# Optimization experiments

Measured on AMD Instinct MI355X. Metric: run time of the kernel, lower is better.

## Reference

```python
import math
import jax, jax.numpy as jnp
import numpy as np

B, LQ, LK, D, H = 4, 2048, 2048, 512, 8  # dim_Q=dim_K=dim_V=D, num_heads=H


def _layernorm(x, g, b, eps=1e-5):
    mu = jnp.mean(x, axis=-1, keepdims=True)
    var = jnp.var(x, axis=-1, keepdims=True)
    return (x - mu) * jax.lax.rsqrt(var + eps) * g + b


def setup_inputs() -> dict:
    key = jax.random.key(0)
    ks = jax.random.split(key, 16)
    s = 1.0 / math.sqrt(D)
    return {
        "Q": jax.random.normal(ks[0], (B, LQ, D), jnp.float32),
        "K": jax.random.normal(ks[1], (B, LK, D), jnp.float32),
        "pad_mask": jax.random.randint(ks[2], (B, LK), 0, 2, jnp.int32),
        "Wq": jax.random.normal(ks[3], (D, D), jnp.float32) * s,
        "bq": jnp.zeros((D,), jnp.float32),
        "Wk": jax.random.normal(ks[4], (D, D), jnp.float32) * s,
        "bk": jnp.zeros((D,), jnp.float32),
        "Wv": jax.random.normal(ks[5], (D, D), jnp.float32) * s,
        "bv": jnp.zeros((D,), jnp.float32),
        "Wo": jax.random.normal(ks[6], (D, D), jnp.float32) * s,
        "bo": jnp.zeros((D,), jnp.float32),
        "g0": jnp.ones((D,), jnp.float32),
        "b0": jnp.zeros((D,), jnp.float32),
        "g1": jnp.ones((D,), jnp.float32),
        "b1": jnp.zeros((D,), jnp.float32),
    }


def reference(Q, K, pad_mask, Wq, bq, Wk, bk, Wv, bv, Wo, bo, g0, b0, g1, b1):
    d = D // H  # head dim (torch: split(dim_split, 2) then cat along batch)
    Qh = (Q @ Wq + bq).reshape(B, LQ, H, d)
    Kh = (K @ Wk + bk).reshape(B, LK, H, d)
    Vh = (K @ Wv + bv).reshape(B, LK, H, d)
    # NOTE: original scales by sqrt(dim_V), not sqrt(head_dim)
    score = jnp.einsum('bqhd,bkhd->bhqk', Qh, Kh) / np.float32(math.sqrt(D))
    m = pad_mask[:, None, None, :].astype(score.dtype)  # (B,1,1,Lk)
    score = jnp.where(m == 0, jnp.float32(-1e12), score)
    A = jax.nn.softmax(score, axis=-1) * m  # post-softmax mask multiply (faithful)
    O = jnp.einsum('bhqk,bkhd->bqhd', A, Vh).reshape(B, LQ, D)
    O = Q + O
    O = _layernorm(O, g0, b0)
    O = O + jax.nn.relu(O @ Wo + bo)
    O = _layernorm(O, g1, b1)
    return O
```

## Files before the change

kernel.cpp:

```cpp
#include <hip/hip_runtime.h>
#include <math.h>

#define NB   4
#define SLQ  2048
#define SLK  2048
#define DIM  512
#define NH   8
#define HD   64
#define NROWS (NB * SLQ)
#define NT   (SLK / 64)

typedef __attribute__((ext_vector_type(8)))  __bf16 bf16x8;
typedef __attribute__((ext_vector_type(4)))  __bf16 bf16x4;
typedef __attribute__((ext_vector_type(2)))  __bf16 bf16x2;
typedef __attribute__((ext_vector_type(4)))  float  f32x4;
typedef __attribute__((ext_vector_type(16))) float  f32x16;
typedef __attribute__((ext_vector_type(4)))  unsigned int u32x4;

typedef const __attribute__((address_space(1))) void* as1_cptr;
typedef __attribute__((address_space(3))) void*       as3_ptr;
__device__ __forceinline__ void async_ld16(const void* g, void* s) {
    __builtin_amdgcn_global_load_lds((as1_cptr)g, (as3_ptr)s, 16, 0, 0);
}

__global__ __launch_bounds__(256)
void transpose_w_kernel(const float* __restrict__ Wq, const float* __restrict__ Wk,
                        const float* __restrict__ Wv, const float* __restrict__ Wo,
                        const int* __restrict__ maskp,
                        __bf16* __restrict__ Wt, float* __restrict__ msentg) {
    const int m = blockIdx.z;
    const int t = threadIdx.x;
    if (m == 4) {
        const int idx = (blockIdx.y * 16 + blockIdx.x) * 256 + t;
        if (idx < NB * SLK) msentg[idx] = maskp[idx] ? 0.f : -1e30f;
        return;
    }
    __shared__ float Ls[32][33];
    const float* W = (m == 0) ? Wq : (m == 1) ? Wk : (m == 2) ? Wv : Wo;
    const int k0 = blockIdx.y * 32, n0 = blockIdx.x * 32;
    const int r  = t >> 3, c = (t & 7) * 4;

    const float4 v = *reinterpret_cast<const float4*>(&W[(size_t)(k0 + r) * DIM + n0 + c]);
    Ls[r][c + 0] = v.x; Ls[r][c + 1] = v.y; Ls[r][c + 2] = v.z; Ls[r][c + 3] = v.w;
    __syncthreads();

    const int n = t >> 3, k = (t & 7) * 4;
    bf16x4 o;
    o[0] = (__bf16)Ls[k + 0][n];
    o[1] = (__bf16)Ls[k + 1][n];
    o[2] = (__bf16)Ls[k + 2][n];
    o[3] = (__bf16)Ls[k + 3][n];
    *reinterpret_cast<bf16x4*>(&Wt[(size_t)(512 * m + n0 + n) * DIM + k0 + k]) = o;
}

__global__ __launch_bounds__(256)
void proj_mfma_kernel(const float* __restrict__ Qp, const float* __restrict__ Kp,
                      const __bf16* __restrict__ Wt,
                      const float* __restrict__ bq, const float* __restrict__ bk,
                      const float* __restrict__ bv,
                      __bf16* __restrict__ Qh, __bf16* __restrict__ Kh,
                      __bf16* __restrict__ VhT) {
    __shared__ __bf16 As[128][72];
    __shared__ __bf16 Bs[64][72];

    const int bx = blockIdx.x;
    const int mode = (bx < 8) ? 0 : (bx < 16) ? 1 : 2;
    const int cb   = bx - ((mode == 0) ? 0 : (mode == 1) ? 8 : 16);
    const float*  A    = (mode == 0) ? Qp : Kp;
    const __bf16* Bt   = Wt + (size_t)((mode == 0) ? 0 : (mode == 1) ? 512 : 1024) * DIM;
    const float*  bias = ((mode == 0) ? bq : (mode == 1) ? bk : bv) + cb * 64;
    const int col0 = cb * 64;

    const int t  = threadIdx.x;
    const int w  = t >> 6, l = t & 63, lg = l >> 4, lc = l & 15;
    const int wr = w >> 1, wc = w & 1;
    const int row0 = blockIdx.y * 128;

    f32x4 acc[4][2];
    #pragma unroll
    for (int mi = 0; mi < 4; ++mi)
        #pragma unroll
        for (int nj = 0; nj < 2; ++nj) acc[mi][nj] = f32x4{0.f, 0.f, 0.f, 0.f};

    const int sr = t >> 3, sc = (t & 7) * 8;

    for (int k0 = 0; k0 < DIM; k0 += 64) {
        __syncthreads();
        #pragma unroll
        for (int i = 0; i < 4; ++i) {
            const int r = i * 32 + sr;
            const float4 a0 = *reinterpret_cast<const float4*>(
                &A[(size_t)(row0 + r) * DIM + k0 + sc]);
            const float4 a1 = *reinterpret_cast<const float4*>(
                &A[(size_t)(row0 + r) * DIM + k0 + sc + 4]);
            bf16x8 hv;
            hv[0] = (__bf16)a0.x; hv[1] = (__bf16)a0.y;
            hv[2] = (__bf16)a0.z; hv[3] = (__bf16)a0.w;
            hv[4] = (__bf16)a1.x; hv[5] = (__bf16)a1.y;
            hv[6] = (__bf16)a1.z; hv[7] = (__bf16)a1.w;
            *reinterpret_cast<bf16x8*>(&As[r][sc]) = hv;
        }
        #pragma unroll
        for (int i = 0; i < 2; ++i) {
            const int n = i * 32 + sr;
            *reinterpret_cast<bf16x8*>(&Bs[n][sc]) =
                *reinterpret_cast<const bf16x8*>(&Bt[(size_t)(col0 + n) * DIM + k0 + sc]);
        }
        __syncthreads();

        #pragma unroll
        for (int ks = 0; ks < 2; ++ks) {
            bf16x8 af[4], bfv[2];
            #pragma unroll
            for (int mi = 0; mi < 4; ++mi)
                af[mi] = *reinterpret_cast<const bf16x8*>(
                    &As[wr * 64 + mi * 16 + lc][ks * 32 + lg * 8]);
            #pragma unroll
            for (int nj = 0; nj < 2; ++nj)
                bfv[nj] = *reinterpret_cast<const bf16x8*>(
                    &Bs[wc * 32 + nj * 16 + lc][ks * 32 + lg * 8]);
            #pragma unroll
            for (int mi = 0; mi < 4; ++mi)
                #pragma unroll
                for (int nj = 0; nj < 2; ++nj)
                    acc[mi][nj] = __builtin_amdgcn_mfma_f32_16x16x32_bf16(
                        af[mi], bfv[nj], acc[mi][nj], 0, 0, 0);
        }
    }

    #pragma unroll
    for (int mi = 0; mi < 4; ++mi) {
        #pragma unroll
        for (int nj = 0; nj < 2; ++nj) {
            const int cl  = wc * 32 + nj * 16 + lc;
            const float bb = bias[cl];
            if (mode == 2) {
                const int dcol = col0 + cl;
                const int hh = dcol >> 6, dd = dcol & 63;
                const int row = row0 + wr * 64 + mi * 16 + lg * 4;
                const int bi  = row >> 11, key = row & 2047;
                bf16x4 pk;
                #pragma unroll
                for (int r = 0; r < 4; ++r) pk[r] = (__bf16)(acc[mi][nj][r] + bb);
                *reinterpret_cast<bf16x4*>(
                    &VhT[((size_t)(bi * NH + hh) * HD + dd) * SLK + key]) = pk;
            } else {
                __bf16* out = (mode == 0) ? Qh : Kh;
                #pragma unroll
                for (int r = 0; r < 4; ++r) {
                    const int row = row0 + wr * 64 + mi * 16 + lg * 4 + r;
                    out[(size_t)row * DIM + col0 + cl] = (__bf16)(acc[mi][nj][r] + bb);
                }
            }
        }
    }
}

__global__ __launch_bounds__(256)
void ffn_mfma_kernel(const __bf16* __restrict__ A, const __bf16* __restrict__ Bt,
                     const float* __restrict__ bias, float* __restrict__ outv) {
    __shared__ __bf16 As[128][72];
    __shared__ __bf16 Bs[64][72];

    const int t  = threadIdx.x;
    const int w  = t >> 6, l = t & 63, lg = l >> 4, lc = l & 15;
    const int wr = w >> 1, wc = w & 1;
    const int row0 = blockIdx.y * 128, col0 = blockIdx.x * 64;

    f32x4 acc[4][2];
    #pragma unroll
    for (int mi = 0; mi < 4; ++mi)
        #pragma unroll
        for (int nj = 0; nj < 2; ++nj) acc[mi][nj] = f32x4{0.f, 0.f, 0.f, 0.f};

    const int sr = t >> 3, sc = (t & 7) * 8;

    for (int k0 = 0; k0 < DIM; k0 += 64) {
        __syncthreads();
        #pragma unroll
        for (int i = 0; i < 4; ++i) {
            const int r = i * 32 + sr;
            *reinterpret_cast<bf16x8*>(&As[r][sc]) =
                *reinterpret_cast<const bf16x8*>(&A[(size_t)(row0 + r) * DIM + k0 + sc]);
        }
        #pragma unroll
        for (int i = 0; i < 2; ++i) {
            const int n = i * 32 + sr;
            *reinterpret_cast<bf16x8*>(&Bs[n][sc]) =
                *reinterpret_cast<const bf16x8*>(&Bt[(size_t)(col0 + n) * DIM + k0 + sc]);
        }
        __syncthreads();

        #pragma unroll
        for (int ks = 0; ks < 2; ++ks) {
            bf16x8 af[4], bfv[2];
            #pragma unroll
            for (int mi = 0; mi < 4; ++mi)
                af[mi] = *reinterpret_cast<const bf16x8*>(
                    &As[wr * 64 + mi * 16 + lc][ks * 32 + lg * 8]);
            #pragma unroll
            for (int nj = 0; nj < 2; ++nj)
                bfv[nj] = *reinterpret_cast<const bf16x8*>(
                    &Bs[wc * 32 + nj * 16 + lc][ks * 32 + lg * 8]);
            #pragma unroll
            for (int mi = 0; mi < 4; ++mi)
                #pragma unroll
                for (int nj = 0; nj < 2; ++nj)
                    acc[mi][nj] = __builtin_amdgcn_mfma_f32_16x16x32_bf16(
                        af[mi], bfv[nj], acc[mi][nj], 0, 0, 0);
        }
    }

    #pragma unroll
    for (int mi = 0; mi < 4; ++mi) {
        #pragma unroll
        for (int nj = 0; nj < 2; ++nj) {
            const int cl  = wc * 32 + nj * 16 + lc;
            const int col = col0 + cl;
            #pragma unroll
            for (int r = 0; r < 4; ++r) {
                const int row = row0 + wr * 64 + mi * 16 + lg * 4 + r;
                const float vv = acc[mi][nj][r] + bias[col];
                outv[(size_t)row * DIM + col] =
                    (float)A[(size_t)row * DIM + col] + fmaxf(vv, 0.f);
            }
        }
    }
}

__global__ __launch_bounds__(256)
void attn_mfma_kernel(const __bf16* __restrict__ Qh, const __bf16* __restrict__ Kh,
                      const __bf16* __restrict__ VhT, const float* __restrict__ msentg,
                      __bf16* __restrict__ Oa) {
    const int pos  = blockIdx.x;
    const int orig = (pos & 7) * 64 + (pos >> 3);
    const int qb = orig & 15;
    const int h  = (orig >> 4) & 7;
    const int b  = orig >> 7;

    const int tid = threadIdx.x;
    const int w   = tid >> 6;
    const int l   = tid & 63;
    const int ql  = l & 31;
    const int hi  = l >> 5;
    const int x7  = ql & 7;

    __shared__ __bf16 Ks[3][64][64];
    __shared__ __bf16 Vt[3][64][64];
    __shared__ float  msent[SLK];
    __shared__ float  linv[4][32];

    {
        const float* mb = msentg + b * SLK;
        #pragma unroll
        for (int i = 0; i < 2; ++i) {
            const int idx = (i * 256 + tid) * 4;
            *reinterpret_cast<f32x4*>(&msent[idx]) =
                *reinterpret_cast<const f32x4*>(&mb[idx]);
        }
    }

    const int q0 = qb * 128 + w * 32;
    bf16x8 qf[4];
    {
        const __bf16* qrow = Qh + (size_t)(b * SLQ + q0 + ql) * DIM + h * HD + hi * 8;
        #pragma unroll
        for (int c = 0; c < 4; ++c)
            qf[c] = *reinterpret_cast<const bf16x8*>(qrow + c * 16);
    }

    const __bf16* kbase = Kh  + (size_t)b * SLK * DIM + h * HD;
    const __bf16* vbase = VhT + (size_t)(b * NH + h) * HD * SLK;

    const int srow = l >> 3;
    const int schk = (l & 7) ^ srow;

    auto STAGE = [&](int nb_, int k0_) {
        #pragma unroll
        for (int i = 0; i < 2; ++i) {
            const int rb = w * 16 + i * 8;
            async_ld16(kbase + (size_t)(k0_ + rb + srow) * DIM + schk * 8,
                       &Ks[nb_][rb][0]);
            async_ld16(vbase + (size_t)(rb + srow) * SLK + k0_ + schk * 8,
                       &Vt[nb_][rb][0]);
        }
    };

    f32x16 oacc[2];
    #pragma unroll
    for (int i = 0; i < 16; ++i) { oacc[0][i] = 0.f; oacc[1][i] = 0.f; }
    float l_part = 0.f;
    const float scale2 = 0.06377551f;

    STAGE(0, 0);
    STAGE(1, 64);
    asm volatile("s_waitcnt lgkmcnt(0)" ::: "memory");

    int rd = 0;
    for (int t = 0; t < NT; ++t) {
        if (t == NT - 1) asm volatile("s_waitcnt vmcnt(0)" ::: "memory");
        else             asm volatile("s_waitcnt vmcnt(4)" ::: "memory");
        __builtin_amdgcn_s_barrier();

        if (t + 2 < NT) {
            const int st = (rd + 2 >= 3) ? rd - 1 : rd + 2;
            STAGE(st, (t + 2) * 64);
        }

        const int k0 = t * 64;
        const __bf16* KsC = &Ks[rd][0][0];
        const __bf16* VtC = &Vt[rd][0][0];

        f32x16 sacc[2];
        #pragma unroll
        for (int i = 0; i < 16; ++i) { sacc[0][i] = 0.f; sacc[1][i] = 0.f; }
        __builtin_amdgcn_s_setprio(1);
        #pragma unroll
        for (int kb = 0; kb < 2; ++kb) {
            #pragma unroll
            for (int c = 0; c < 4; ++c) {
                const bf16x8 kf = *reinterpret_cast<const bf16x8*>(
                    &KsC[(kb * 32 + ql) * 64 + (((2 * c + hi) ^ x7) << 3)]);
                sacc[kb] = __builtin_amdgcn_mfma_f32_32x32x16_bf16(
                    kf, qf[c], sacc[kb], 0, 0, 0);
            }
        }
        __builtin_amdgcn_s_setprio(0);

        unsigned int P2[2][8];
        #pragma unroll
        for (int kb = 0; kb < 2; ++kb) {
            #pragma unroll
            for (int m = 0; m < 4; ++m) {
                const f32x4 tm = *reinterpret_cast<const f32x4*>(
                    &msent[k0 + kb * 32 + 8 * m + 4 * hi]);
                float p[4];
                #pragma unroll
                for (int j = 0; j < 4; ++j) {
                    p[j] = __builtin_amdgcn_exp2f(
                        fmaf(sacc[kb][4 * m + j], scale2, tm[j]));
                    l_part += p[j];
                }
                bf16x2 w0, w1;
                w0[0] = (__bf16)p[0]; w0[1] = (__bf16)p[1];
                w1[0] = (__bf16)p[2]; w1[1] = (__bf16)p[3];
                P2[kb][2 * m]     = __builtin_bit_cast(unsigned int, w0);
                P2[kb][2 * m + 1] = __builtin_bit_cast(unsigned int, w1);
            }
        }

        #pragma unroll
        for (int kb = 0; kb < 2; ++kb) {
            #pragma unroll
            for (int cc = 0; cc < 2; ++cc) {
                asm volatile("v_permlane32_swap_b32 %0, %1"
                             : "+v"(P2[kb][4 * cc + 0]), "+v"(P2[kb][4 * cc + 2]));
                asm volatile("v_permlane32_swap_b32 %0, %1"
                             : "+v"(P2[kb][4 * cc + 1]), "+v"(P2[kb][4 * cc + 3]));
            }
        }
        bf16x8 pfrag[4];
        #pragma unroll
        for (int c = 0; c < 4; ++c) {
            const int kb = c >> 1, cc = c & 1;
            u32x4 fw;
            fw.x = P2[kb][4 * cc + 0]; fw.y = P2[kb][4 * cc + 1];
            fw.z = P2[kb][4 * cc + 2]; fw.w = P2[kb][4 * cc + 3];
            pfrag[c] = __builtin_bit_cast(bf16x8, fw);
        }

        __builtin_amdgcn_s_setprio(1);
        #pragma unroll
        for (int db = 0; db < 2; ++db) {
            #pragma unroll
            for (int c = 0; c < 4; ++c) {
                const bf16x8 vf = *reinterpret_cast<const bf16x8*>(
                    &VtC[(db * 32 + ql) * 64 + (((2 * c + hi) ^ x7) << 3)]);
                oacc[db] = __builtin_amdgcn_mfma_f32_32x32x16_bf16(
                    pfrag[c], vf, oacc[db], 0, 0, 0);
            }
        }
        __builtin_amdgcn_s_setprio(0);

        rd = (rd == 2) ? 0 : rd + 1;
    }

    const float lsum = l_part + __shfl_xor(l_part, 32, 64);
    if (hi == 0) linv[w][ql] = (lsum > 0.f) ? 1.f / lsum : 0.f;
    #pragma unroll
    for (int db = 0; db < 2; ++db) {
        #pragma unroll
        for (int m = 0; m < 4; ++m) {
            const f32x4 iv = *reinterpret_cast<const f32x4*>(&linv[w][8 * m + 4 * hi]);
            #pragma unroll
            for (int j = 0; j < 4; ++j) {
                const int qr = 8 * m + 4 * hi + j;
                Oa[(size_t)(b * SLQ + q0 + qr) * DIM + h * HD + db * 32 + ql] =
                    (__bf16)(oacc[db][4 * m + j] * iv[j]);
            }
        }
    }
}

__device__ __forceinline__ float wave_sum(float v) {
    #pragma unroll
    for (int off = 32; off > 0; off >>= 1) v += __shfl_xor(v, off, 64);
    return v;
}

__global__ __launch_bounds__(256)
void ln1_kernel(const __bf16* X, const float* Y,
                const float* g, const float* bta, __bf16* out) {
    const int w    = threadIdx.x >> 6;
    const int lane = threadIdx.x & 63;
    const int row  = blockIdx.x * 4 + w;
    const size_t base = (size_t)row * DIM + lane * 8;

    const bf16x8 xv = *reinterpret_cast<const bf16x8*>(&X[base]);
    const float4 y0 = *reinterpret_cast<const float4*>(&Y[base]);
    const float4 y1 = *reinterpret_cast<const float4*>(&Y[base + 4]);
    float v[8];
    v[0] = (float)xv[0] + y0.x; v[1] = (float)xv[1] + y0.y;
    v[2] = (float)xv[2] + y0.z; v[3] = (float)xv[3] + y0.w;
    v[4] = (float)xv[4] + y1.x; v[5] = (float)xv[5] + y1.y;
    v[6] = (float)xv[6] + y1.z; v[7] = (float)xv[7] + y1.w;

    float s = 0.f, ss = 0.f;
    #pragma unroll
    for (int i = 0; i < 8; ++i) { s += v[i]; ss += v[i] * v[i]; }
    s  = wave_sum(s);
    ss = wave_sum(ss);
    const float mean = s * (1.f / DIM);
    const float var  = ss * (1.f / DIM) - mean * mean;
    const float rstd = rsqrtf(var + 1e-5f);

    const float4 g0 = *reinterpret_cast<const float4*>(&g[lane * 8]);
    const float4 g1 = *reinterpret_cast<const float4*>(&g[lane * 8 + 4]);
    const float4 b0 = *reinterpret_cast<const float4*>(&bta[lane * 8]);
    const float4 b1 = *reinterpret_cast<const float4*>(&bta[lane * 8 + 4]);
    float gg[8] = {g0.x, g0.y, g0.z, g0.w, g1.x, g1.y, g1.z, g1.w};
    float bb[8] = {b0.x, b0.y, b0.z, b0.w, b1.x, b1.y, b1.z, b1.w};

    bf16x8 o;
    #pragma unroll
    for (int i = 0; i < 8; ++i)
        o[i] = (__bf16)((v[i] - mean) * rstd * gg[i] + bb[i]);
    *reinterpret_cast<bf16x8*>(&out[base]) = o;
}

__global__ __launch_bounds__(256)
void ln2_kernel(const float* X, const float* g, const float* bta, float* out) {
    const int w    = threadIdx.x >> 6;
    const int lane = threadIdx.x & 63;
    const int row  = blockIdx.x * 4 + w;
    const size_t base = (size_t)row * DIM + lane * 8;

    float v[8];
    *reinterpret_cast<float4*>(&v[0]) = *reinterpret_cast<const float4*>(&X[base]);
    *reinterpret_cast<float4*>(&v[4]) = *reinterpret_cast<const float4*>(&X[base + 4]);

    float s = 0.f, ss = 0.f;
    #pragma unroll
    for (int i = 0; i < 8; ++i) { s += v[i]; ss += v[i] * v[i]; }
    s  = wave_sum(s);
    ss = wave_sum(ss);
    const float mean = s * (1.f / DIM);
    const float var  = ss * (1.f / DIM) - mean * mean;
    const float rstd = rsqrtf(var + 1e-5f);

    const float4 g0 = *reinterpret_cast<const float4*>(&g[lane * 8]);
    const float4 g1 = *reinterpret_cast<const float4*>(&g[lane * 8 + 4]);
    const float4 b0 = *reinterpret_cast<const float4*>(&bta[lane * 8]);
    const float4 b1 = *reinterpret_cast<const float4*>(&bta[lane * 8 + 4]);
    float gg[8] = {g0.x, g0.y, g0.z, g0.w, g1.x, g1.y, g1.z, g1.w};
    float bb[8] = {b0.x, b0.y, b0.z, b0.w, b1.x, b1.y, b1.z, b1.w};

    float4 o0, o1;
    o0.x = (v[0] - mean) * rstd * gg[0] + bb[0];
    o0.y = (v[1] - mean) * rstd * gg[1] + bb[1];
    o0.z = (v[2] - mean) * rstd * gg[2] + bb[2];
    o0.w = (v[3] - mean) * rstd * gg[3] + bb[3];
    o1.x = (v[4] - mean) * rstd * gg[4] + bb[4];
    o1.y = (v[5] - mean) * rstd * gg[5] + bb[5];
    o1.z = (v[6] - mean) * rstd * gg[6] + bb[6];
    o1.w = (v[7] - mean) * rstd * gg[7] + bb[7];
    *reinterpret_cast<float4*>(&out[base])     = o0;
    *reinterpret_cast<float4*>(&out[base + 4]) = o1;
}

extern "C" void kernel_launch(void* const* d_in, const int* in_sizes, int n_in,
                              void* d_out, int out_size, void* d_ws, size_t ws_size,
                              hipStream_t stream) {
    const float* Q     = (const float*)d_in[0];
    const float* K     = (const float*)d_in[1];
    const int*   maskp = (const int*)  d_in[2];
    const float* Wq    = (const float*)d_in[3];
    const float* bq    = (const float*)d_in[4];
    const float* Wk    = (const float*)d_in[5];
    const float* bk    = (const float*)d_in[6];
    const float* Wv    = (const float*)d_in[7];
    const float* bv    = (const float*)d_in[8];
    const float* Wo    = (const float*)d_in[9];
    const float* bo    = (const float*)d_in[10];
    const float* g0    = (const float*)d_in[11];
    const float* b0    = (const float*)d_in[12];
    const float* g1    = (const float*)d_in[13];
    const float* b1    = (const float*)d_in[14];

    float* out = (float*)d_out;
    char*  ws  = (char*)d_ws;
    __bf16* Qh     = (__bf16*)ws;
    __bf16* Kh     = (__bf16*)(ws + (8u  << 20));
    __bf16* VhT    = (__bf16*)(ws + (16u << 20));
    __bf16* Wt     = (__bf16*)(ws + (24u << 20));
    __bf16* Oa     = (__bf16*)(ws + (26u << 20));
    __bf16* H1     = (__bf16*)(ws + (34u << 20));
    float*  msentg = (float*)(ws + (42u << 20));
    float*  R2     = (float*)ws;

    transpose_w_kernel<<<dim3(16, 16, 5), 256, 0, stream>>>(
        Wq, Wk, Wv, Wo, maskp, Wt, msentg);

    proj_mfma_kernel<<<dim3(24, 64), 256, 0, stream>>>(
        Q, K, Wt, bq, bk, bv, Qh, Kh, VhT);

    attn_mfma_kernel<<<dim3(512), 256, 0, stream>>>(Qh, Kh, VhT, msentg, Oa);

    ln1_kernel<<<NROWS / 4, 256, 0, stream>>>(Oa, Q, g0, b0, H1);

    ffn_mfma_kernel<<<dim3(8, 64), 256, 0, stream>>>(
        H1, Wt + (size_t)1536 * DIM, bo, R2);

    ln2_kernel<<<NROWS / 4, 256, 0, stream>>>(R2, g1, b1, out);
}
```

Measured before the change: 145.1 us.

## Widen projection tiles with async swizzled B loads; store FFN output as bf16

The projection GEMM now computes 128x128 tiles instead of 128x64, halving the grid and the number of times each A tile is read and converted from fp32. Weight tiles are loaded straight into LDS with global_load_lds and an XOR swizzle to avoid bank conflicts. Separately, the FFN residual output is stored as bf16 rather than fp32, halving that intermediate's traffic into the second layernorm at some cost in precision. The wider tile doubles accumulator registers, which may lower occupancy.

```diff
diff --git a/kernel.cpp b/kernel.cpp
--- a/kernel.cpp
+++ b/kernel.cpp
@@ -61,28 +61,31 @@
                       __bf16* __restrict__ Qh, __bf16* __restrict__ Kh,
                       __bf16* __restrict__ VhT) {
     __shared__ __bf16 As[128][72];
-    __shared__ __bf16 Bs[64][72];
-
-    const int bx = blockIdx.x;
-    const int mode = (bx < 8) ? 0 : (bx < 16) ? 1 : 2;
-    const int cb   = bx - ((mode == 0) ? 0 : (mode == 1) ? 8 : 16);
+    __shared__ __bf16 Bs[128][64];
+
+    const int bx   = blockIdx.x;
+    const int mode = bx >> 2;
+    const int cb   = bx & 3;
     const float*  A    = (mode == 0) ? Qp : Kp;
-    const __bf16* Bt   = Wt + (size_t)((mode == 0) ? 0 : (mode == 1) ? 512 : 1024) * DIM;
-    const float*  bias = ((mode == 0) ? bq : (mode == 1) ? bk : bv) + cb * 64;
-    const int col0 = cb * 64;
+    const __bf16* Bt   = Wt + (size_t)(mode * 512) * DIM;
+    const float*  bias = ((mode == 0) ? bq : (mode == 1) ? bk : bv) + cb * 128;
+    const int col0 = cb * 128;
 
     const int t  = threadIdx.x;
     const int w  = t >> 6, l = t & 63, lg = l >> 4, lc = l & 15;
     const int wr = w >> 1, wc = w & 1;
     const int row0 = blockIdx.y * 128;
 
-    f32x4 acc[4][2];
+    f32x4 acc[4][4];
     #pragma unroll
     for (int mi = 0; mi < 4; ++mi)
         #pragma unroll
-        for (int nj = 0; nj < 2; ++nj) acc[mi][nj] = f32x4{0.f, 0.f, 0.f, 0.f};
-
-    const int sr = t >> 3, sc = (t & 7) * 8;
+        for (int nj = 0; nj < 4; ++nj) acc[mi][nj] = f32x4{0.f, 0.f, 0.f, 0.f};
+
+    const int sr   = t >> 3, sc = (t & 7) * 8;
+    const int srow = l >> 3;
+    const int schk = (l & 7) ^ srow;
+    const int x7   = lc & 7;
 
     for (int k0 = 0; k0 < DIM; k0 += 64) {
         __syncthreads();
@@ -101,28 +104,30 @@
             *reinterpret_cast<bf16x8*>(&As[r][sc]) = hv;
         }
         #pragma unroll
-        for (int i = 0; i < 2; ++i) {
-            const int n = i * 32 + sr;
-            *reinterpret_cast<bf16x8*>(&Bs[n][sc]) =
-                *reinterpret_cast<const bf16x8*>(&Bt[(size_t)(col0 + n) * DIM + k0 + sc]);
+        for (int i = 0; i < 4; ++i) {
+            const int rb = w * 32 + i * 8;
+            async_ld16(Bt + (size_t)(col0 + rb + srow) * DIM + k0 + schk * 8,
+                       &Bs[rb][0]);
         }
         __syncthreads();
 
         #pragma unroll
         for (int ks = 0; ks < 2; ++ks) {
-            bf16x8 af[4], bfv[2];
+            bf16x8 af[4], bfv[4];
             #pragma unroll
             for (int mi = 0; mi < 4; ++mi)
                 af[mi] = *reinterpret_cast<const bf16x8*>(
                     &As[wr * 64 + mi * 16 + lc][ks * 32 + lg * 8]);
             #pragma unroll
-            for (int nj = 0; nj < 2; ++nj)
+            for (int nj = 0; nj < 4; ++nj) {
+                const int rowb = wc * 64 + nj * 16 + lc;
                 bfv[nj] = *reinterpret_cast<const bf16x8*>(
-                    &Bs[wc * 32 + nj * 16 + lc][ks * 32 + lg * 8]);
+                    &Bs[rowb][(((ks * 4 + lg) ^ x7) << 3)]);
+            }
             #pragma unroll
             for (int mi = 0; mi < 4; ++mi)
                 #pragma unroll
-                for (int nj = 0; nj < 2; ++nj)
+                for (int nj = 0; nj < 4; ++nj)
                     acc[mi][nj] = __builtin_amdgcn_mfma_f32_16x16x32_bf16(
                         af[mi], bfv[nj], acc[mi][nj], 0, 0, 0);
         }
@@ -131,8 +136,8 @@
     #pragma unroll
     for (int mi = 0; mi < 4; ++mi) {
         #pragma unroll
-        for (int nj = 0; nj < 2; ++nj) {
-            const int cl  = wc * 32 + nj * 16 + lc;
+        for (int nj = 0; nj < 4; ++nj) {
+            const int cl  = wc * 64 + nj * 16 + lc;
             const float bb = bias[cl];
             if (mode == 2) {
                 const int dcol = col0 + cl;
@@ -158,7 +163,7 @@
 
 __global__ __launch_bounds__(256)
 void ffn_mfma_kernel(const __bf16* __restrict__ A, const __bf16* __restrict__ Bt,
-                     const float* __restrict__ bias, float* __restrict__ outv) {
+                     const float* __restrict__ bias, __bf16* __restrict__ outv) {
     __shared__ __bf16 As[128][72];
     __shared__ __bf16 Bs[64][72];
 
@@ -222,7 +227,7 @@
                 const int row = row0 + wr * 64 + mi * 16 + lg * 4 + r;
                 const float vv = acc[mi][nj][r] + bias[col];
                 outv[(size_t)row * DIM + col] =
-                    (float)A[(size_t)row * DIM + col] + fmaxf(vv, 0.f);
+                    (__bf16)((float)A[(size_t)row * DIM + col] + fmaxf(vv, 0.f));
             }
         }
     }
@@ -449,15 +454,16 @@
 }
 
 __global__ __launch_bounds__(256)
-void ln2_kernel(const float* X, const float* g, const float* bta, float* out) {
+void ln2_kernel(const __bf16* X, const float* g, const float* bta, float* out) {
     const int w    = threadIdx.x >> 6;
     const int lane = threadIdx.x & 63;
     const int row  = blockIdx.x * 4 + w;
     const size_t base = (size_t)row * DIM + lane * 8;
 
+    const bf16x8 xv = *reinterpret_cast<const bf16x8*>(&X[base]);
     float v[8];
-    *reinterpret_cast<float4*>(&v[0]) = *reinterpret_cast<const float4*>(&X[base]);
-    *reinterpret_cast<float4*>(&v[4]) = *reinterpret_cast<const float4*>(&X[base + 4]);
+    #pragma unroll
+    for (int i = 0; i < 8; ++i) v[i] = (float)xv[i];
 
     float s = 0.f, ss = 0.f;
     #pragma unroll
@@ -516,12 +522,12 @@
     __bf16* Oa     = (__bf16*)(ws + (26u << 20));
     __bf16* H1     = (__bf16*)(ws + (34u << 20));
     float*  msentg = (float*)(ws + (42u << 20));
-    float*  R2     = (float*)ws;
+    __bf16* R2     = (__bf16*)ws;
 
     transpose_w_kernel<<<dim3(16, 16, 5), 256, 0, stream>>>(
         Wq, Wk, Wv, Wo, maskp, Wt, msentg);
 
-    proj_mfma_kernel<<<dim3(24, 64), 256, 0, stream>>>(
+    proj_mfma_kernel<<<dim3(12, 64), 256, 0, stream>>>(
         Q, K, Wt, bq, bk, bv, Qh, Kh, VhT);
 
     attn_mfma_kernel<<<dim3(512), 256, 0, stream>>>(Qh, Kh, VhT, msentg, Oa);
```

Measured after the change: 138.7 us. -4.4%, faster.
